# Kernel optimization log

Measured on AMD Instinct MI355X. Metric: run time of the kernel, lower is better.

Reference implementation:

```python
import jax, jax.numpy as jnp
import numpy as np

NUM_HEADS = 16
ROPE_BASE = 10000.0
QK_GAIN_INIT = 12.0
EPS = 1e-6
# head_config = alternating ['rope','nope',...]; 1.0 -> RoPE applied to this head
ROPE_MASK = jnp.asarray(np.tile([1.0, 0.0], NUM_HEADS // 2), dtype=jnp.float32)


def setup_inputs() -> dict:
    key = jax.random.key(0)
    k0, k1, k2 = jax.random.split(key, 3)
    B, S, Dm = 2, 2048, 2048
    x = jax.random.normal(k0, (B, S, Dm), dtype=jnp.float32)
    # fused QKV projection and output projection (out_proj flagged zero-init in the
    # original; we use small random init so outputs/grads are non-trivial)
    w_qkv = jax.random.normal(k1, (Dm, 3 * Dm), dtype=jnp.float32) * (Dm ** -0.5)
    w_out = jax.random.normal(k2, (Dm, Dm), dtype=jnp.float32) * (Dm ** -0.5)
    q_gain = jnp.full((NUM_HEADS,), QK_GAIN_INIT, dtype=jnp.float32)
    return {"x": x, "w_qkv": w_qkv, "w_out": w_out, "q_gain": q_gain}


def _rope_cos_sin(seqlen, head_dim, dtype):
    half = head_dim // 2
    inv_freq = ROPE_BASE ** (-jnp.arange(0, half, dtype=jnp.float32) / half)
    theta = jnp.arange(seqlen, dtype=jnp.float32)[:, None] * inv_freq[None, :]  # [S, D/2]
    return jnp.cos(theta).astype(dtype), jnp.sin(theta).astype(dtype)


def _apply_rope(t, cos, sin):
    # t: [B, S, H, D]; cos/sin: [S, D/2] -> broadcast [1, S, 1, D/2]
    d2 = t.shape[-1] // 2
    t1, t2 = t[..., :d2], t[..., d2:]
    c = cos[None, :, None, :]
    s = sin[None, :, None, :]
    return jnp.concatenate([t1 * c - t2 * s, t1 * s + t2 * c], axis=-1)


def _unit_norm(t):
    # per-head-dim L2 normalization (qk-norm)
    return t * jax.lax.rsqrt(jnp.sum(t * t, axis=-1, keepdims=True) + EPS)


def reference(x, w_qkv, w_out, q_gain):
    B, S, Dm = x.shape
    H = NUM_HEADS
    D = Dm // H
    qkv = (x @ w_qkv).reshape(B, S, 3, H, D)
    q, k, v = qkv[:, :, 0], qkv[:, :, 1], qkv[:, :, 2]  # [B, S, H, D]
    q = _unit_norm(q)
    k = _unit_norm(k)
    cos, sin = _rope_cos_sin(S, D, x.dtype)
    m = ROPE_MASK[None, None, :, None]  # heterogeneous per-head dispatch
    q = m * _apply_rope(q, cos, sin) + (1.0 - m) * q
    k = m * _apply_rope(k, cos, sin) + (1.0 - m) * k
    # per-head learned qk gain instead of 1/sqrt(d)
    logits = jnp.einsum('bshd,bthd->bhst', q, k) * q_gain[None, :, None, None]
    causal = jnp.tril(jnp.ones((S, S), dtype=bool))
    logits = jnp.where(causal[None, None], logits, jnp.finfo(logits.dtype).min)
    attn = jax.nn.softmax(logits, axis=-1)
    y = jnp.einsum('bhst,bthd->bshd', attn, v).reshape(B, S, Dm)
    return y @ w_out
```

## Files before the change

kernel.cpp:

```cpp
#include <hip/hip_runtime.h>
#include <hip/hip_bf16.h>

typedef unsigned short ushort_t;
typedef __attribute__((ext_vector_type(8))) short short8;
typedef __attribute__((ext_vector_type(4))) float floatx4;

#define B_  2
#define S_  2048
#define DM_ 2048
#define H_  16
#define DH_ 128

#define AS1(p) ((const __attribute__((address_space(1))) void*)(p))
#define AS3(p) ((__attribute__((address_space(3))) void*)(p))

static __device__ __forceinline__ float b2f(ushort_t u) {
  __hip_bfloat16 h = *reinterpret_cast<__hip_bfloat16*>(&u);
  return __bfloat162float(h);
}
static __device__ __forceinline__ ushort_t f2b(float f) {
  __hip_bfloat16 h = __float2bfloat16(f);
  return *reinterpret_cast<ushort_t*>(&h);
}
static __device__ __forceinline__ float fast_exp2(float x) {
#if defined(__has_builtin)
#if __has_builtin(__builtin_amdgcn_exp2f)
  return __builtin_amdgcn_exp2f(x);
#else
  return exp2f(x);
#endif
#else
  return exp2f(x);
#endif
}

static __device__ __forceinline__ void transpose_body(const float* __restrict__ in,
                                                      ushort_t* __restrict__ out,
                                                      int R, int inC, int colOff,
                                                      int bx, int by,
                                                      ushort_t (*tile)[72], int tid) {
  const int r0 = by * 64, c0 = bx * 64;
#pragma unroll
  for (int p = 0; p < 2; ++p) {
    int li = tid + p * 256;
    int r = li >> 3, cs = (li & 7) * 8;
    const float* src = in + (size_t)(r0 + r) * inC + colOff + c0 + cs;
    float4 a = *(const float4*)src;
    float4 b = *(const float4*)(src + 4);
    ushort_t tmp[8] = {f2b(a.x), f2b(a.y), f2b(a.z), f2b(a.w),
                       f2b(b.x), f2b(b.y), f2b(b.z), f2b(b.w)};
    *(uint4*)&tile[r][cs] = *(const uint4*)tmp;
  }
  __syncthreads();
#pragma unroll
  for (int p = 0; p < 2; ++p) {
    int li = tid + p * 256;
    int cR = li >> 3, rs = (li & 7) * 8;
    ushort_t tmp[8];
#pragma unroll
    for (int e = 0; e < 8; ++e) tmp[e] = tile[rs + e][cR];
    *(uint4*)(out + (size_t)(c0 + cR) * R + r0 + rs) = *(const uint4*)tmp;
  }
}

__global__ __launch_bounds__(256) void fused_pre(const float* __restrict__ x,
                                                 const float* __restrict__ w_qkv,
                                                 ushort_t* __restrict__ xbf,
                                                 ushort_t* __restrict__ wqkT,
                                                 ushort_t* __restrict__ wvT) {
  __shared__ ushort_t tile[64][72];
  const int bid = blockIdx.x;
  const int tid = threadIdx.x;
  if (bid < 4096) {
    size_t i = ((size_t)bid * 256 + tid) * 8;
    float4 a = *(const float4*)(x + i);
    float4 b = *(const float4*)(x + i + 4);
    ushort_t tmp[8] = {f2b(a.x), f2b(a.y), f2b(a.z), f2b(a.w),
                       f2b(b.x), f2b(b.y), f2b(b.z), f2b(b.w)};
    *(uint4*)(xbf + i) = *(const uint4*)tmp;
    return;
  }
  if (bid < 6144) {
    int t = bid - 4096;
    transpose_body(w_qkv, wqkT, DM_, 3 * DM_, 0, t & 63, t >> 6, tile, tid);
  } else {
    int t = bid - 6144;
    transpose_body(w_qkv, wvT, DM_, 3 * DM_, 2 * DM_, t & 31, t >> 5, tile, tid);
  }
}

#define SBAR() __builtin_amdgcn_sched_barrier(0)
#define BARR() __builtin_amdgcn_s_barrier()

#define LDS_A(qm, bb)                                                          \
  _Pragma("unroll") for (int mi = 0; mi < 4; ++mi) {                           \
    _Pragma("unroll") for (int ks = 0; ks < 2; ++ks) {                         \
      const int r_ = arow + (qm) * 64 + mi * 16;                               \
      const int cb_ = ((ks) * 64 + quad * 16) ^ swz;                           \
      afr[qm][mi][ks] =                                                        \
          *(const short8*)((const char*)As[bb] + r_ * 128 + cb_);              \
    }                                                                          \
  }

#define LDS_B(qn, bb)                                                          \
  _Pragma("unroll") for (int ni = 0; ni < 2; ++ni) {                           \
    _Pragma("unroll") for (int ks = 0; ks < 2; ++ks) {                         \
      const int r_ = brow + (qn) * 32 + ni * 16;                               \
      const int cb_ = ((ks) * 64 + quad * 16) ^ swz;                           \
      bfr[qn][ni][ks] =                                                        \
          *(const short8*)((const char*)Bs[bb] + r_ * 128 + cb_);              \
    }                                                                          \
  }

#define MMA_Q(qm, qn)                                                          \
  _Pragma("unroll") for (int mi = 0; mi < 4; ++mi) {                           \
    _Pragma("unroll") for (int ni = 0; ni < 2; ++ni) {                         \
      floatx4 t_ = acc[(qm) * 4 + mi][(qn) * 2 + ni];                          \
      t_ = __builtin_amdgcn_mfma_f32_16x16x32_bf16(afr[qm][mi][0],             \
                                                   bfr[qn][ni][0], t_, 0, 0, 0); \
      t_ = __builtin_amdgcn_mfma_f32_16x16x32_bf16(afr[qm][mi][1],             \
                                                   bfr[qn][ni][1], t_, 0, 0, 0); \
      acc[(qm) * 4 + mi][(qn) * 2 + ni] = t_;                                  \
    }                                                                          \
  }

template <int MODE>
__global__ __launch_bounds__(512, 2) void gemm_bt_256(const ushort_t* __restrict__ A,
                                                      const ushort_t* __restrict__ Bt,
                                                      void* __restrict__ C0,
                                                      void* __restrict__ C1,
                                                      int M, int N, int K) {
  __shared__ alignas(16) ushort_t As[2][256 * 64];
  __shared__ alignas(16) ushort_t Bs[2][256 * 64];
  const int tid = threadIdx.x;
  const int wave = tid >> 6, lane = tid & 63;
  const int l15 = lane & 15, quad = lane >> 4;
  const int wm = wave >> 2, wn = wave & 3;
  const size_t m0 = (size_t)blockIdx.y * 256, n0 = (size_t)blockIdx.x * 256;
  const int nkt = K >> 6;

  const int srow = lane >> 3;
  const int skk = ((lane & 7) ^ srow) * 8;

  const int arow = wm * 128 + l15;
  const int brow = wn * 64 + l15;
  const int swz = (l15 & 7) << 4;

  floatx4 zero = {0.f, 0.f, 0.f, 0.f};
  floatx4 acc[8][4];
#pragma unroll
  for (int i = 0; i < 8; ++i)
#pragma unroll
    for (int j = 0; j < 4; ++j) acc[i][j] = zero;

  short8 afr[2][4][2];
  short8 bfr[2][2][2];

  auto stage_half = [&](int t, int ht) {
    if (t >= nkt) return;
    const int bb = t & 1;
    const int h = ht & 1;
    const int kt64 = t << 6;
    const ushort_t* G = (ht < 2) ? A : Bt;
    const size_t r0 = (ht < 2) ? m0 : n0;
    char* dst = (char*)((ht < 2) ? As[bb] : Bs[bb]) + h * 16384;
#pragma unroll
    for (int i = 0; i < 2; ++i) {
      const int c = wave * 2 + i;
      const size_t gr = r0 + h * 128 + c * 8 + srow;
      __builtin_amdgcn_global_load_lds(AS1(G + gr * K + kt64 + skk),
                                       AS3(dst + c * 1024), 16, 0, 0);
    }
  };

  stage_half(0, 0); stage_half(0, 1); stage_half(0, 2); stage_half(0, 3);
  stage_half(1, 0); stage_half(1, 1);
  SBAR();
  if (nkt > 1) { asm volatile("s_waitcnt vmcnt(4)" ::: "memory"); }
  else         { asm volatile("s_waitcnt vmcnt(0)" ::: "memory"); }
  SBAR(); BARR(); SBAR();

  for (int kt = 0; kt < nkt; ++kt) {
    const int bb = kt & 1;
    LDS_A(0, bb); LDS_B(0, bb);
    stage_half(kt + 1, 2);
    SBAR();
    __builtin_amdgcn_s_setprio(1);
    MMA_Q(0, 0);
    __builtin_amdgcn_s_setprio(0);
    SBAR();
    LDS_A(1, bb);
    stage_half(kt + 1, 3);
    SBAR();
    __builtin_amdgcn_s_setprio(1);
    MMA_Q(1, 0);
    __builtin_amdgcn_s_setprio(0);
    SBAR(); BARR(); SBAR();
    LDS_B(1, bb);
    stage_half(kt + 2, 0);
    SBAR();
    __builtin_amdgcn_s_setprio(1);
    MMA_Q(1, 1);
    __builtin_amdgcn_s_setprio(0);
    SBAR();
    stage_half(kt + 2, 1);
    SBAR();
    __builtin_amdgcn_s_setprio(1);
    MMA_Q(0, 1);
    __builtin_amdgcn_s_setprio(0);
    SBAR();
    if (kt + 2 < nkt) { asm volatile("s_waitcnt vmcnt(4)" ::: "memory"); }
    else              { asm volatile("s_waitcnt vmcnt(0)" ::: "memory"); }
    SBAR(); BARR(); SBAR();
  }

  if (MODE == 2) {
    ushort_t* Cb = (n0 >= 2048) ? (ushort_t*)C1 : (ushort_t*)C0;
    size_t nc0 = n0 & 2047;
#pragma unroll
    for (int mi8 = 0; mi8 < 8; ++mi8)
#pragma unroll
      for (int nj = 0; nj < 4; ++nj)
#pragma unroll
        for (int r = 0; r < 4; ++r) {
          size_t row = m0 + wm * 128 + (mi8 >> 2) * 64 + (mi8 & 3) * 16 + quad * 4 + r;
          size_t col = nc0 + wn * 64 + (nj >> 1) * 32 + (nj & 1) * 16 + l15;
          Cb[row * 2048 + col] = f2b(acc[mi8][nj][r]);
        }
  } else {
#pragma unroll
    for (int mi8 = 0; mi8 < 8; ++mi8)
#pragma unroll
      for (int nj = 0; nj < 4; ++nj)
#pragma unroll
        for (int r = 0; r < 4; ++r) {
          size_t row = m0 + wm * 128 + (mi8 >> 2) * 64 + (mi8 & 3) * 16 + quad * 4 + r;
          size_t col = n0 + wn * 64 + (nj >> 1) * 32 + (nj & 1) * 16 + l15;
          if (MODE == 1)
            ((float*)C0)[row * N + col] = acc[mi8][nj][r];
          else
            ((ushort_t*)C0)[row * N + col] = f2b(acc[mi8][nj][r]);
        }
  }
}

#define LDS_A8(mh, bb)                                                         \
  _Pragma("unroll") for (int mi = 0; mi < 2; ++mi) {                           \
    _Pragma("unroll") for (int ks = 0; ks < 2; ++ks) {                         \
      const int r_ = arow + ((mh) * 2 + mi) * 16;                              \
      const int cb_ = ((ks) * 64 + quad * 16) ^ swz;                           \
      afr[(mh) * 2 + mi][ks] =                                                 \
          *(const short8*)((const char*)As[bb] + r_ * 128 + cb_);              \
    }                                                                          \
  }

#define LDS_B8(nh, bb)                                                         \
  _Pragma("unroll") for (int ni = 0; ni < 2; ++ni) {                           \
    _Pragma("unroll") for (int ks = 0; ks < 2; ++ks) {                         \
      const int r_ = brow + ((nh) * 2 + ni) * 16;                              \
      const int cb_ = ((ks) * 64 + quad * 16) ^ swz;                           \
      bfr[(nh) * 2 + ni][ks] =                                                 \
          *(const short8*)((const char*)Bs[bb] + r_ * 128 + cb_);              \
    }                                                                          \
  }

#define MMA_H(mh, nh)                                                          \
  _Pragma("unroll") for (int mi = 0; mi < 2; ++mi) {                           \
    _Pragma("unroll") for (int ni = 0; ni < 2; ++ni) {                         \
      floatx4 t_ = acc[(mh) * 2 + mi][(nh) * 2 + ni];                          \
      t_ = __builtin_amdgcn_mfma_f32_16x16x32_bf16(afr[(mh) * 2 + mi][0],      \
                                                   bfr[(nh) * 2 + ni][0], t_, 0, 0, 0); \
      t_ = __builtin_amdgcn_mfma_f32_16x16x32_bf16(afr[(mh) * 2 + mi][1],      \
                                                   bfr[(nh) * 2 + ni][1], t_, 0, 0, 0); \
      acc[(mh) * 2 + mi][(nh) * 2 + ni] = t_;                                  \
    }                                                                          \
  }

template <int MODE>
__global__ __launch_bounds__(256, 2) void gemm_bt_128(const ushort_t* __restrict__ A,
                                                      const ushort_t* __restrict__ Bt,
                                                      void* __restrict__ C0,
                                                      int M, int N, int K) {
  __shared__ alignas(16) ushort_t As[2][128 * 64];
  __shared__ alignas(16) ushort_t Bs[2][128 * 64];
  const int tid = threadIdx.x;
  const int wave = tid >> 6, lane = tid & 63;
  const int l15 = lane & 15, quad = lane >> 4;
  const int wm = wave >> 1, wn = wave & 1;
  const int lin = blockIdx.y * gridDim.x + blockIdx.x;
  const int band = lin / (4 * gridDim.x);
  const int rin = lin % (4 * gridDim.x);
  const int by = band * 4 + (rin & 3);
  const int bx = rin >> 2;
  const size_t m0 = (size_t)by * 128, n0 = (size_t)bx * 128;
  const int nkt = K >> 6;

  const int srow = lane >> 3;
  const int skk = ((lane & 7) ^ srow) * 8;

  const int arow = wm * 64 + l15;
  const int brow = wn * 64 + l15;
  const int swz = (l15 & 7) << 4;

  floatx4 zero = {0.f, 0.f, 0.f, 0.f};
  floatx4 acc[4][4];
#pragma unroll
  for (int i = 0; i < 4; ++i)
#pragma unroll
    for (int j = 0; j < 4; ++j) acc[i][j] = zero;

  short8 afr[4][2];
  short8 bfr[4][2];

  auto stage_q = [&](int t, int qt_) {
    if (t >= nkt) return;
    const int bb = t & 1;
    const int h = qt_ & 1;
    const int kt64 = t << 6;
    const ushort_t* G = (qt_ < 2) ? A : Bt;
    const size_t r0 = (qt_ < 2) ? m0 : n0;
    char* dst = (char*)((qt_ < 2) ? As[bb] : Bs[bb]) + h * 8192;
#pragma unroll
    for (int i = 0; i < 2; ++i) {
      const int c = wave * 2 + i;
      const size_t gr = r0 + h * 64 + c * 8 + srow;
      __builtin_amdgcn_global_load_lds(AS1(G + gr * K + kt64 + skk),
                                       AS3(dst + c * 1024), 16, 0, 0);
    }
  };

  stage_q(0, 0); stage_q(0, 1); stage_q(0, 2); stage_q(0, 3);
  stage_q(1, 0); stage_q(1, 1);
  SBAR();
  if (nkt > 1) { asm volatile("s_waitcnt vmcnt(4)" ::: "memory"); }
  else         { asm volatile("s_waitcnt vmcnt(0)" ::: "memory"); }
  SBAR(); BARR(); SBAR();

  for (int kt = 0; kt < nkt; ++kt) {
    const int bb = kt & 1;
    LDS_A8(0, bb); LDS_B8(0, bb);
    stage_q(kt + 1, 2);
    SBAR();
    __builtin_amdgcn_s_setprio(1);
    MMA_H(0, 0);
    __builtin_amdgcn_s_setprio(0);
    SBAR();
    LDS_A8(1, bb);
    stage_q(kt + 1, 3);
    SBAR();
    __builtin_amdgcn_s_setprio(1);
    MMA_H(1, 0);
    __builtin_amdgcn_s_setprio(0);
    SBAR(); BARR(); SBAR();
    LDS_B8(1, bb);
    stage_q(kt + 2, 0);
    SBAR();
    __builtin_amdgcn_s_setprio(1);
    MMA_H(1, 1);
    __builtin_amdgcn_s_setprio(0);
    SBAR();
    stage_q(kt + 2, 1);
    SBAR();
    __builtin_amdgcn_s_setprio(1);
    MMA_H(0, 1);
    __builtin_amdgcn_s_setprio(0);
    SBAR();
    if (kt + 2 < nkt) { asm volatile("s_waitcnt vmcnt(4)" ::: "memory"); }
    else              { asm volatile("s_waitcnt vmcnt(0)" ::: "memory"); }
    SBAR(); BARR(); SBAR();
  }

#pragma unroll
  for (int i = 0; i < 4; ++i)
#pragma unroll
    for (int j = 0; j < 4; ++j)
#pragma unroll
      for (int r = 0; r < 4; ++r) {
        size_t row = m0 + wm * 64 + i * 16 + quad * 4 + r;
        size_t col = n0 + wn * 64 + j * 16 + l15;
        if (MODE == 1)
          ((float*)C0)[row * N + col] = acc[i][j][r];
        else
          ((ushort_t*)C0)[row * N + col] = f2b(acc[i][j][r]);
      }
}

__global__ __launch_bounds__(256) void fused_mid(ushort_t* __restrict__ Q,
                                                 ushort_t* __restrict__ Kb,
                                                 const float* __restrict__ gain,
                                                 const float* __restrict__ w_out,
                                                 ushort_t* __restrict__ woutT) {
  __shared__ ushort_t tile[64][72];
  const int bid = blockIdx.x;
  const int tid = threadIdx.x;
  if (bid >= 4096) {
    int t = bid - 4096;
    transpose_body(w_out, woutT, DM_, DM_, 0, t & 31, t >> 5, tile, tid);
    return;
  }
  const int wave = tid >> 6, lane = tid & 63;
  const int g16 = lane >> 4, sl = lane & 15;
  const int idx = (bid * 4 + wave) * 4 + g16;
  const int h = idx & 15;
  const int s = (idx >> 4) & (S_ - 1);
  const size_t off = (size_t)(idx >> 4) * DM_ + h * DH_ + sl * 4;

  ushort_t qv1[4], qv2[4], kv1[4], kv2[4];
  *(uint2*)qv1 = *(const uint2*)(Q + off);
  *(uint2*)qv2 = *(const uint2*)(Q + off + 64);
  *(uint2*)kv1 = *(const uint2*)(Kb + off);
  *(uint2*)kv2 = *(const uint2*)(Kb + off + 64);

  float q1[4], q2[4], k1[4], k2[4];
  float sq = 0.f, sk = 0.f;
#pragma unroll
  for (int e = 0; e < 4; ++e) {
    q1[e] = b2f(qv1[e]); q2[e] = b2f(qv2[e]);
    k1[e] = b2f(kv1[e]); k2[e] = b2f(kv2[e]);
    sq += q1[e] * q1[e] + q2[e] * q2[e];
    sk += k1[e] * k1[e] + k2[e] * k2[e];
  }
#pragma unroll
  for (int o = 1; o < 16; o <<= 1) {
    sq += __shfl_xor(sq, o, 64);
    sk += __shfl_xor(sk, o, 64);
  }
  float rq = rsqrtf(sq + 1e-6f), rk = rsqrtf(sk + 1e-6f);
  const float g = gain[h] * 1.44269504f;
  const bool roped = (h & 1) == 0;
#pragma unroll
  for (int e = 0; e < 4; ++e) {
    float a = q1[e] * rq, bq = q2[e] * rq;
    float c_ = k1[e] * rk, dk = k2[e] * rk;
    if (roped) {
      int j = sl * 4 + e;
      float invf = exp2f((float)j * -0.20762050593f);
      float th = (float)s * invf;
      float cc = cosf(th), sn = sinf(th);
      float na = a * cc - bq * sn, nb = a * sn + bq * cc;
      float nc = c_ * cc - dk * sn, nd = c_ * sn + dk * cc;
      a = na; bq = nb; c_ = nc; dk = nd;
    }
    qv1[e] = f2b(a * g); qv2[e] = f2b(bq * g);
    kv1[e] = f2b(c_);    kv2[e] = f2b(dk);
  }
  *(uint2*)(Q + off)       = *(const uint2*)qv1;
  *(uint2*)(Q + off + 64)  = *(const uint2*)qv2;
  *(uint2*)(Kb + off)      = *(const uint2*)kv1;
  *(uint2*)(Kb + off + 64) = *(const uint2*)kv2;
}

__global__ __launch_bounds__(256, 2) void attn(ushort_t* __restrict__ QY,
                                               const ushort_t* __restrict__ Kg,
                                               const ushort_t* __restrict__ Vg) {
  __shared__ alignas(16) ushort_t Ks[2][64 * 128];
  __shared__ alignas(16) ushort_t Vs[2][128 * 64];
  __shared__ alignas(16) ushort_t Ps[2][4][16 * 64];

  const float M0 = 18.755035531f;
  const int tid = threadIdx.x;
  const int wave = tid >> 6, lane = tid & 63;
  const int l15 = lane & 15, quad = lane >> 4;
  const int bh = blockIdx.x;
  const int b = bh >> 4, h = bh & 15;
  const int p = blockIdx.y;
  const int qt[2] = {p, 31 - p};

  const ushort_t* Kgb = Kg + (size_t)b * S_ * DM_ + h * DH_;
  const ushort_t* Vgb = Vg + (size_t)(h * DH_) * (B_ * S_) + b * S_;

  short8 aq[2][4];
#pragma unroll
  for (int t = 0; t < 2; ++t) {
    const ushort_t* Qg =
        QY + (size_t)(b * S_ + qt[t] * 64 + wave * 16 + l15) * DM_ + h * DH_;
#pragma unroll
    for (int ks = 0; ks < 4; ++ks)
      aq[t][ks] = *(const short8*)(Qg + ks * 32 + quad * 8);
  }

  float lsum[2][4] = {{0.f, 0.f, 0.f, 0.f}, {0.f, 0.f, 0.f, 0.f}};
  floatx4 zero = {0.f, 0.f, 0.f, 0.f};
  floatx4 oacc[2][8];
#pragma unroll
  for (int t = 0; t < 2; ++t)
#pragma unroll
    for (int d = 0; d < 8; ++d) oacc[t][d] = zero;

  const int krow_in = lane >> 4, ksd = lane & 15;
  const int vrow_in = lane >> 3, vsd = lane & 7;

  auto stage = [&](int kt, int bf) {
#pragma unroll
    for (int i = 0; i < 4; ++i) {
      int c = wave * 4 + i;
      {
        int r = c * 4 + krow_in;
        int sg = ksd ^ (r & 7);
        __builtin_amdgcn_global_load_lds(
            AS1(Kgb + (size_t)(kt * 64 + r) * DM_ + sg * 8),
            AS3((char*)Ks[bf] + c * 1024), 16, 0, 0);
      }
      {
        int r = c * 8 + vrow_in;
        int sg = vsd ^ (r & 7);
        __builtin_amdgcn_global_load_lds(
            AS1(Vgb + (size_t)r * (B_ * S_) + kt * 64 + sg * 8),
            AS3((char*)Vs[bf] + c * 1024), 16, 0, 0);
      }
    }
  };

  stage(0, 0);

  for (int kt = 0; kt <= qt[1]; ++kt) {
    const int cur = kt & 1;
    __syncthreads();
    if (kt < qt[1]) stage(kt + 1, cur ^ 1);

#pragma unroll
    for (int t = 0; t < 2; ++t) {
      if (t == 0 && kt > qt[0]) continue;
      floatx4 sacc[4];
#pragma unroll
      for (int j = 0; j < 4; ++j) sacc[j] = zero;
#pragma unroll
      for (int ks = 0; ks < 4; ++ks) {
#pragma unroll
        for (int j = 0; j < 4; ++j) {
          int row = j * 16 + l15;
          int sl = (ks * 4 + quad) ^ (row & 7);
          short8 bk = *(const short8*)&Ks[cur][row * 128 + sl * 8];
          sacc[j] = __builtin_amdgcn_mfma_f32_16x16x32_bf16(aq[t][ks], bk, sacc[j], 0, 0, 0);
        }
      }
      if (kt == qt[t]) {
#pragma unroll
        for (int j = 0; j < 4; ++j)
#pragma unroll
          for (int r = 0; r < 4; ++r) {
            int key = j * 16 + l15;
            int qr = wave * 16 + quad * 4 + r;
            if (key > qr) sacc[j][r] = -1e30f;
          }
      }
#pragma unroll
      for (int j = 0; j < 4; ++j)
#pragma unroll
        for (int r = 0; r < 4; ++r) {
          float pv = fast_exp2(sacc[j][r] - M0);
          sacc[j][r] = pv;
          lsum[t][r] += pv;
        }
#pragma unroll
      for (int j = 0; j < 4; ++j)
#pragma unroll
        for (int r = 0; r < 4; ++r) {
          int row = quad * 4 + r;
          int col = j * 16 + l15;
          int g = col >> 3, w = col & 7;
          Ps[t][wave][row * 64 + ((g ^ (row & 7)) << 3) + w] = f2b(sacc[j][r]);
        }
#pragma unroll
      for (int ks2 = 0; ks2 < 2; ++ks2) {
        short8 ap = *(const short8*)&Ps[t][wave][l15 * 64 +
                                                (((ks2 * 4 + quad) ^ (l15 & 7)) << 3)];
#pragma unroll
        for (int d = 0; d < 8; ++d) {
          int row = d * 16 + l15;
          int sl = (ks2 * 4 + quad) ^ (row & 7);
          short8 bv = *(const short8*)&Vs[cur][row * 64 + sl * 8];
          oacc[t][d] = __builtin_amdgcn_mfma_f32_16x16x32_bf16(ap, bv, oacc[t][d], 0, 0, 0);
        }
      }
    }
  }

#pragma unroll
  for (int t = 0; t < 2; ++t) {
#pragma unroll
    for (int r = 0; r < 4; ++r) {
#pragma unroll
      for (int o = 1; o < 16; o <<= 1) lsum[t][r] += __shfl_xor(lsum[t][r], o, 64);
      float inv = 1.0f / lsum[t][r];
      size_t row = (size_t)(b * S_ + qt[t] * 64 + wave * 16 + quad * 4 + r);
#pragma unroll
      for (int d = 0; d < 8; ++d) {
        size_t col = (size_t)h * DH_ + d * 16 + l15;
        QY[row * DM_ + col] = f2b(oacc[t][d][r] * inv);
      }
    }
  }
}

extern "C" void kernel_launch(void* const* d_in, const int* in_sizes, int n_in,
                              void* d_out, int out_size, void* d_ws, size_t ws_size,
                              hipStream_t stream) {
  const float* x      = (const float*)d_in[0];
  const float* w_qkv  = (const float*)d_in[1];
  const float* w_out  = (const float*)d_in[2];
  const float* q_gain = (const float*)d_in[3];
  float* out = (float*)d_out;

  char* ws = (char*)d_ws;
  const size_t bsd = (size_t)B_ * S_ * DM_;
  ushort_t* Qraw = (ushort_t*)ws;
  ushort_t* Kraw = Qraw + bsd;
  ushort_t* Vt   = Kraw + bsd;
  ushort_t* wvT  = Vt + bsd;
  ushort_t* xbf  = (ushort_t*)d_out;
  ushort_t* wqkT = xbf + bsd;
  ushort_t* woutT = wvT;

  fused_pre<<<dim3(7168), 256, 0, stream>>>(x, w_qkv, xbf, wqkT, wvT);
  gemm_bt_256<2><<<dim3(16, 16), 512, 0, stream>>>(xbf, wqkT, Qraw, Kraw,
                                                   B_ * S_, 2 * DM_, DM_);
  gemm_bt_128<0><<<dim3(32, 16), 256, 0, stream>>>(wvT, xbf, Vt,
                                                   DM_, B_ * S_, DM_);
  fused_mid<<<dim3(5120), 256, 0, stream>>>(Qraw, Kraw, q_gain, w_out, woutT);
  attn<<<dim3(B_ * H_, S_ / 128), 256, 0, stream>>>(Qraw, Kraw, Vt);
  gemm_bt_128<1><<<dim3(16, 32), 256, 0, stream>>>(Qraw, woutT, out,
                                                   B_ * S_, DM_, DM_);
}
```

Measured before the change: 342.2 us.

## Make each wave row-group stage its own A half and drop a mid-iteration barrier

In both GEMM kernels, the A-tile halves are now loaded only by the waves whose wm index consumes that half, with each of those waves issuing four loads instead of two. B loading stays shared across all waves. Because each A half is produced and consumed by the same wave group, the block-wide barrier in the middle of the k-loop is removed, cutting synchronization stalls. The risk is that waves now issue uneven numbers of memory ops, so the fixed vmcnt(4) waits may no longer match the outstanding-load counts. Cross-wave visibility of LDS writes without the barrier is also a correctness risk.

```diff
diff --git a/kernel.cpp b/kernel.cpp
--- a/kernel.cpp
+++ b/kernel.cpp
@@ -156,25 +156,36 @@
   short8 afr[2][4][2];
   short8 bfr[2][2][2];
 
-  auto stage_half = [&](int t, int ht) {
+  auto stage_B = [&](int t, int h) {
     if (t >= nkt) return;
     const int bb = t & 1;
-    const int h = ht & 1;
     const int kt64 = t << 6;
-    const ushort_t* G = (ht < 2) ? A : Bt;
-    const size_t r0 = (ht < 2) ? m0 : n0;
-    char* dst = (char*)((ht < 2) ? As[bb] : Bs[bb]) + h * 16384;
+    char* dst = (char*)Bs[bb] + h * 16384;
 #pragma unroll
     for (int i = 0; i < 2; ++i) {
       const int c = wave * 2 + i;
-      const size_t gr = r0 + h * 128 + c * 8 + srow;
-      __builtin_amdgcn_global_load_lds(AS1(G + gr * K + kt64 + skk),
+      const size_t gr = n0 + h * 128 + c * 8 + srow;
+      __builtin_amdgcn_global_load_lds(AS1(Bt + gr * K + kt64 + skk),
                                        AS3(dst + c * 1024), 16, 0, 0);
     }
   };
-
-  stage_half(0, 0); stage_half(0, 1); stage_half(0, 2); stage_half(0, 3);
-  stage_half(1, 0); stage_half(1, 1);
+  auto stage_A = [&](int t, int h) {
+    if (t >= nkt || wm != h) return;
+    const int bb = t & 1;
+    const int kt64 = t << 6;
+    char* dst = (char*)As[bb] + h * 16384;
+#pragma unroll
+    for (int i = 0; i < 4; ++i) {
+      const int c = (wave & 3) * 4 + i;
+      const size_t gr = m0 + h * 128 + c * 8 + srow;
+      __builtin_amdgcn_global_load_lds(AS1(A + gr * K + kt64 + skk),
+                                       AS3(dst + c * 1024), 16, 0, 0);
+    }
+  };
+
+  stage_B(0, 0); stage_B(0, 1);
+  stage_A(0, 0); stage_A(0, 1);
+  stage_A(1, 0); stage_A(1, 1);
   SBAR();
   if (nkt > 1) { asm volatile("s_waitcnt vmcnt(4)" ::: "memory"); }
   else         { asm volatile("s_waitcnt vmcnt(0)" ::: "memory"); }
@@ -183,27 +194,27 @@
   for (int kt = 0; kt < nkt; ++kt) {
     const int bb = kt & 1;
     LDS_A(0, bb); LDS_B(0, bb);
-    stage_half(kt + 1, 2);
+    stage_B(kt + 1, 0);
     SBAR();
     __builtin_amdgcn_s_setprio(1);
     MMA_Q(0, 0);
     __builtin_amdgcn_s_setprio(0);
     SBAR();
     LDS_A(1, bb);
-    stage_half(kt + 1, 3);
+    stage_B(kt + 1, 1);
     SBAR();
     __builtin_amdgcn_s_setprio(1);
     MMA_Q(1, 0);
     __builtin_amdgcn_s_setprio(0);
-    SBAR(); BARR(); SBAR();
+    SBAR();
     LDS_B(1, bb);
-    stage_half(kt + 2, 0);
+    stage_A(kt + 2, 0);
     SBAR();
     __builtin_amdgcn_s_setprio(1);
     MMA_Q(1, 1);
     __builtin_amdgcn_s_setprio(0);
     SBAR();
-    stage_half(kt + 2, 1);
+    stage_A(kt + 2, 1);
     SBAR();
     __builtin_amdgcn_s_setprio(1);
     MMA_Q(0, 1);
@@ -312,25 +323,36 @@
   short8 afr[4][2];
   short8 bfr[4][2];
 
-  auto stage_q = [&](int t, int qt_) {
+  auto stage_B = [&](int t, int h) {
     if (t >= nkt) return;
     const int bb = t & 1;
-    const int h = qt_ & 1;
     const int kt64 = t << 6;
-    const ushort_t* G = (qt_ < 2) ? A : Bt;
-    const size_t r0 = (qt_ < 2) ? m0 : n0;
-    char* dst = (char*)((qt_ < 2) ? As[bb] : Bs[bb]) + h * 8192;
+    char* dst = (char*)Bs[bb] + h * 8192;
 #pragma unroll
     for (int i = 0; i < 2; ++i) {
       const int c = wave * 2 + i;
-      const size_t gr = r0 + h * 64 + c * 8 + srow;
-      __builtin_amdgcn_global_load_lds(AS1(G + gr * K + kt64 + skk),
+      const size_t gr = n0 + h * 64 + c * 8 + srow;
+      __builtin_amdgcn_global_load_lds(AS1(Bt + gr * K + kt64 + skk),
                                        AS3(dst + c * 1024), 16, 0, 0);
     }
   };
-
-  stage_q(0, 0); stage_q(0, 1); stage_q(0, 2); stage_q(0, 3);
-  stage_q(1, 0); stage_q(1, 1);
+  auto stage_A = [&](int t, int h) {
+    if (t >= nkt || wm != h) return;
+    const int bb = t & 1;
+    const int kt64 = t << 6;
+    char* dst = (char*)As[bb] + h * 8192;
+#pragma unroll
+    for (int i = 0; i < 4; ++i) {
+      const int c = (wave & 1) * 4 + i;
+      const size_t gr = m0 + h * 64 + c * 8 + srow;
+      __builtin_amdgcn_global_load_lds(AS1(A + gr * K + kt64 + skk),
+                                       AS3(dst + c * 1024), 16, 0, 0);
+    }
+  };
+
+  stage_B(0, 0); stage_B(0, 1);
+  stage_A(0, 0); stage_A(0, 1);
+  stage_A(1, 0); stage_A(1, 1);
   SBAR();
   if (nkt > 1) { asm volatile("s_waitcnt vmcnt(4)" ::: "memory"); }
   else         { asm volatile("s_waitcnt vmcnt(0)" ::: "memory"); }
@@ -339,27 +361,27 @@
   for (int kt = 0; kt < nkt; ++kt) {
     const int bb = kt & 1;
     LDS_A8(0, bb); LDS_B8(0, bb);
-    stage_q(kt + 1, 2);
+    stage_B(kt + 1, 0);
     SBAR();
     __builtin_amdgcn_s_setprio(1);
     MMA_H(0, 0);
     __builtin_amdgcn_s_setprio(0);
     SBAR();
     LDS_A8(1, bb);
-    stage_q(kt + 1, 3);
+    stage_B(kt + 1, 1);
     SBAR();
     __builtin_amdgcn_s_setprio(1);
     MMA_H(1, 0);
     __builtin_amdgcn_s_setprio(0);
-    SBAR(); BARR(); SBAR();
+    SBAR();
     LDS_B8(1, bb);
-    stage_q(kt + 2, 0);
+    stage_A(kt + 2, 0);
     SBAR();
     __builtin_amdgcn_s_setprio(1);
     MMA_H(1, 1);
     __builtin_amdgcn_s_setprio(0);
     SBAR();
-    stage_q(kt + 2, 1);
+    stage_A(kt + 2, 1);
     SBAR();
     __builtin_amdgcn_s_setprio(1);
     MMA_H(0, 1);
```

Result: no change. 338.8 us (-1.0%).
